# Optimization experiments

Hardware: AMD Instinct MI355X
Metric: run time of the kernel (lower is better)

Reference implementation:

```python
import jax, jax.numpy as jnp
import numpy as np

N_WIN = 7
DIM = 128
QK = 128
HEADS = 8
TOPK = 4


def _win(x, n_win):
    # (N, H, W, C) -> (N, n_win*n_win, h, w, C)
    N, H, W, C = x.shape
    h, w = H // n_win, W // n_win
    return x.reshape(N, n_win, h, n_win, w, C).transpose(0, 1, 3, 2, 4, 5).reshape(N, n_win * n_win, h, w, C)


def _unwin(x, n_win):
    # (N, p2, h, w, C) -> (N, H, W, C)
    N, p2, h, w, C = x.shape
    return x.reshape(N, n_win, n_win, h, w, C).transpose(0, 1, 3, 2, 4, 5).reshape(N, n_win * h, n_win * w, C)


def _dwconv(img_nhwc, k, b):
    # depthwise 3x3, SAME padding (LePE)
    x = img_nhwc.transpose(0, 3, 1, 2)
    y = jax.lax.conv_general_dilated(x, k, (1, 1), 'SAME',
                                     dimension_numbers=('NCHW', 'OIHW', 'NCHW'),
                                     feature_group_count=k.shape[0])
    y = y + b[None, :, None, None]
    return y.transpose(0, 2, 3, 1)


def _branch(xw, W, b):
    # xw: (N, p2, h, w, C); QKV linear + pixel/window-level views
    qkv = xw @ W + b
    q, kv = qkv[..., :QK], qkv[..., QK:]
    N, p2, h, w, _ = q.shape
    q_pix = q.reshape(N, p2, h * w, QK)
    kv_pix = kv.reshape(N, p2, h * w, QK + DIM)  # identity kv_down
    q_win = q.mean((2, 3))
    k_win = kv[..., :QK].mean((2, 3))
    return q_pix, kv_pix, q_win, k_win, kv


def _route(q_win, k_win, scale):
    # non-differentiable routing (detach) with Identity emb
    q = jax.lax.stop_gradient(q_win)
    k = jax.lax.stop_gradient(k_win)
    logit = (q * scale) @ k.transpose(0, 2, 1)  # (N, p2, p2)
    top_val, top_idx = jax.lax.top_k(logit, TOPK)
    r_weight = jax.nn.softmax(top_val, axis=-1)  # unused (mul_weight='none')
    return r_weight, top_idx


def _gather(kv_pix, idx):
    # kv_pix: (N, p2, w2, c), idx: (N, p2, K) -> (N, p2, K, w2, c)
    N = kv_pix.shape[0]
    bidx = jnp.arange(N)[:, None, None]
    return kv_pix[bidx, idx]


def _heads_q(q):
    # (N, p2, w2, m*c) -> (N, p2, m, w2, c)
    N, p2, w2, _ = q.shape
    return q.reshape(N, p2, w2, HEADS, -1).transpose(0, 1, 3, 2, 4)


def _heads_kv(kv):
    # (N, p2, K, w2, m*c) -> (N, p2, m, K*w2, c)
    N, p2, K, w2, _ = kv.shape
    return kv.reshape(N, p2, K, w2, HEADS, -1).transpose(0, 1, 4, 2, 3, 5).reshape(N, p2, HEADS, K * w2, -1)


def setup_inputs() -> dict:
    key = jax.random.key(0)
    ks = jax.random.split(key, 6)
    N, H, W = 8, 56, 56
    return {
        'x': jax.random.normal(ks[0], (N, H, W, DIM), jnp.float32),
        'y': jax.random.normal(ks[1], (N, H, W, DIM), jnp.float32),
        'w_qkv_x': jax.random.normal(ks[2], (DIM, 2 * QK + DIM), jnp.float32) * 0.02,
        'b_qkv_x': jnp.zeros((2 * QK + DIM,), jnp.float32),
        'w_qkv_y': jax.random.normal(ks[3], (DIM, 2 * QK + DIM), jnp.float32) * 0.02,
        'b_qkv_y': jnp.zeros((2 * QK + DIM,), jnp.float32),
        'w_lepe_x': jax.random.normal(ks[4], (DIM, 1, 3, 3), jnp.float32) * 0.1,
        'b_lepe_x': jnp.zeros((DIM,), jnp.float32),
        'w_lepe_y': jax.random.normal(ks[5], (DIM, 1, 3, 3), jnp.float32) * 0.1,
        'b_lepe_y': jnp.zeros((DIM,), jnp.float32),
    }


def reference(x, y, w_qkv_x, b_qkv_x, w_qkv_y, b_qkv_y, w_lepe_x, b_lepe_x, w_lepe_y, b_lepe_y):
    scale = QK ** (-0.5)
    N, H, W, C = x.shape
    h, w = H // N_WIN, W // N_WIN
    xw = _win(x, N_WIN)
    yw = _win(y, N_WIN)

    qx_pix, kvx_pix, qx_win, kx_win, kvx = _branch(xw, w_qkv_x, b_qkv_x)
    qy_pix, kvy_pix, qy_win, ky_win, kvy = _branch(yw, w_qkv_y, b_qkv_y)

    lepe_x = _dwconv(_unwin(kvx[..., QK:], N_WIN), w_lepe_x, b_lepe_x)
    lepe_y = _dwconv(_unwin(kvy[..., QK:], N_WIN), w_lepe_y, b_lepe_y)

    _, rx_idx = _route(qx_win, kx_win, scale)
    _, ry_idx = _route(qy_win, ky_win, scale)

    kvx_sel = _gather(kvx_pix, rx_idx)  # (N, p2, K, w2, QK+DIM)
    kvy_sel = _gather(kvy_pix, ry_idx)

    kx_sel, vx_sel = _heads_kv(kvx_sel[..., :QK]), _heads_kv(kvx_sel[..., QK:])
    ky_sel, vy_sel = _heads_kv(kvy_sel[..., :QK]), _heads_kv(kvy_sel[..., QK:])
    qx = _heads_q(qx_pix)
    qy = _heads_q(qy_pix)

    attn_x = jax.nn.softmax(jnp.einsum('bpmqc,bpmkc->bpmqk', qx * scale, kx_sel), axis=-1)
    attn_y = jax.nn.softmax(jnp.einsum('bpmqc,bpmkc->bpmqk', qy * scale, ky_sel), axis=-1)

    # cross attention: x-output uses y's attention weights on x's values, and vice versa
    out_x = jnp.einsum('bpmqk,bpmkc->bpmqc', attn_y, vx_sel)
    out_y = jnp.einsum('bpmqk,bpmkc->bpmqc', attn_x, vy_sel)

    p2 = N_WIN * N_WIN
    out_x = out_x.transpose(0, 1, 3, 2, 4).reshape(N, p2, h, w, DIM)
    out_y = out_y.transpose(0, 1, 3, 2, 4).reshape(N, p2, h, w, DIM)
    out_x = _unwin(out_x, N_WIN) + lepe_x
    out_y = _unwin(out_y, N_WIN) + lepe_y
    return (out_x, out_y)
```

## Files before the change

### kernel.cpp

```cpp
#include <hip/hip_runtime.h>

#define HWD 56
#define NWIN 7
#define P2 49
#define CIN 128
#define COUT 384
#define NB 8
#define SCALE 0.08838834764831843f

typedef __attribute__((ext_vector_type(8))) short bf16x8;
typedef __attribute__((ext_vector_type(4))) float f32x4;
typedef __attribute__((ext_vector_type(8))) unsigned short u16x8;
typedef unsigned short ushort_t;

#if __has_builtin(__builtin_amdgcn_mfma_f32_16x16x16bf16_1k)
#define HAVE_MFMA16 1
typedef __attribute__((ext_vector_type(4))) short bf16x4;
#endif

__device__ inline unsigned short f2bf(float f) {
  unsigned int u = __float_as_uint(f);
  unsigned int r = (u + 0x7fffu + ((u >> 16) & 1u)) >> 16;
  return (unsigned short)r;
}
__device__ inline float bf2f(unsigned short b) {
  return __uint_as_float(((unsigned int)b) << 16);
}

__global__ __launch_bounds__(256) void meanproj_kernel(
    const float* __restrict__ xin, const float* __restrict__ yin,
    const float* __restrict__ Wx, const float* __restrict__ Bx,
    const float* __restrict__ Wy, const float* __restrict__ By,
    ushort_t* __restrict__ xbfx, ushort_t* __restrict__ xbfy,
    ushort_t* __restrict__ Wtx, ushort_t* __restrict__ Wty,
    float* __restrict__ qwx, float* __restrict__ kwx,
    float* __restrict__ qwy, float* __restrict__ kwy)
{
  const int n = blockIdx.x, p = blockIdx.y, br = blockIdx.z;
  const float* X  = br ? yin : xin;
  const float* W  = br ? Wy  : Wx;
  const float* Bv = br ? By  : Bx;
  ushort_t* xb = (br ? xbfy : xbfx) + (size_t)(n * P2 + p) * 64 * CIN;
  ushort_t* Wt = br ? Wty : Wtx;
  float* qw = br ? qwy : qwx;
  float* kw = br ? kwy : kwx;

  __shared__ float smf[8][132];
  __shared__ float mxs[128];
  const int t = threadIdx.x;
  const int wr = p / NWIN, wc = p % NWIN;
  const int ch4 = (t & 31) * 4, pg = t >> 5;

  const float* Xrow = X + (((size_t)n * HWD + wr * 8 + pg) * HWD + wc * 8) * CIN;
  float4 s4 = {0.f, 0.f, 0.f, 0.f};
#pragma unroll
  for (int i = 0; i < 8; ++i) {
    float4 v = *(const float4*)&Xrow[i * CIN + ch4];
    s4.x += v.x; s4.y += v.y; s4.z += v.z; s4.w += v.w;
    ushort4 o = {f2bf(v.x), f2bf(v.y), f2bf(v.z), f2bf(v.w)};
    *(ushort4*)&xb[(pg * 8 + i) * CIN + ch4] = o;
  }
  *(float4*)&smf[pg][ch4] = s4;
  __syncthreads();
  if (t < 128) {
    float s = 0.f;
#pragma unroll
    for (int g = 0; g < 8; ++g) s += smf[g][t];
    mxs[t] = s * (1.f / 64.f);
  }
  __syncthreads();

  float acc = Bv[t];
#pragma unroll 8
  for (int k = 0; k < 128; ++k) acc = fmaf(mxs[k], W[(size_t)k * COUT + t], acc);
  if (t < 128) qw[(n * P2 + p) * 128 + t] = acc;
  else         kw[(n * P2 + p) * 128 + (t - 128)] = acc;

  if (p == 0) {
    for (int e = t; e < 48 * 128; e += 256) {
      int c = n * 48 + (e >> 7), k = e & 127;
      Wt[(size_t)c * 128 + k] = f2bf(W[(size_t)k * COUT + c]);
    }
  }
}

__global__ __launch_bounds__(256) void route_kernel(
    const float* __restrict__ qwx, const float* __restrict__ kwx,
    const float* __restrict__ qwy, const float* __restrict__ kwy,
    int* __restrict__ idxx, int* __restrict__ idxy)
{
  const int br = blockIdx.x, n = blockIdx.y;
  const float* qw = br ? qwy : qwx;
  const float* kw = br ? kwy : kwx;
  int* idx = br ? idxy : idxx;

  __shared__ float qs[P2][128];
  __shared__ float ks[P2][128];
  __shared__ float ls[P2][52];
  const int t = threadIdx.x;
  for (int e = t; e < P2 * 128; e += 256) {
    qs[e >> 7][e & 127] = qw[(size_t)n * P2 * 128 + e];
    ks[e >> 7][e & 127] = kw[(size_t)n * P2 * 128 + e];
  }
  __syncthreads();
  for (int pair = t; pair < P2 * P2; pair += 256) {
    int r = pair / P2, j = pair % P2;
    float d = 0.f;
#pragma unroll
    for (int c4 = 0; c4 < 32; ++c4) {
      float4 a = *(const float4*)&qs[r][c4 * 4];
      float4 b = *(const float4*)&ks[j][c4 * 4];
      d = fmaf(a.x, b.x, d); d = fmaf(a.y, b.y, d);
      d = fmaf(a.z, b.z, d); d = fmaf(a.w, b.w, d);
    }
    ls[r][j] = d;
  }
  __syncthreads();
  const int lane = t & 63, wv = t >> 6;
  for (int row = wv; row < P2; row += 4) {
    float v = (lane < P2) ? ls[row][lane] : -1e30f;
    int out4[4];
#pragma unroll
    for (int sel = 0; sel < 4; ++sel) {
      float m = v;
#pragma unroll
      for (int msk = 1; msk < 64; msk <<= 1) m = fmaxf(m, __shfl_xor(m, msk));
      unsigned long long b = __ballot(v == m);
      int bi = __ffsll((unsigned long long)b) - 1;
      out4[sel] = bi;
      if (lane == bi) v = -1e30f;
    }
    if (lane == 0) {
      int4 o = {out4[0], out4[1], out4[2], out4[3]};
      *(int4*)&idx[((size_t)n * P2 + row) * 4] = o;
    }
  }
}

#define XS 136
__global__ __launch_bounds__(256) void qkv_gemm_kernel(
    const ushort_t* __restrict__ xbfx, const ushort_t* __restrict__ xbfy,
    const ushort_t* __restrict__ Wtx, const ushort_t* __restrict__ Wty,
    const float* __restrict__ Bx, const float* __restrict__ By,
    ushort_t* __restrict__ Qpx, ushort_t* __restrict__ Qpy,
    ushort_t* __restrict__ Kpx, ushort_t* __restrict__ Kpy,
    ushort_t* __restrict__ Vcx, ushort_t* __restrict__ Vcy,
    ushort_t* __restrict__ Vpx, ushort_t* __restrict__ Vpy)
{
  const int n = blockIdx.x, p = blockIdx.y, br = blockIdx.z;
  const ushort_t* Xw = (br ? xbfy : xbfx) + (size_t)(n * P2 + p) * 64 * CIN;
  const ushort_t* Wt = br ? Wty : Wtx;
  const float* Bv = br ? By : Bx;
  ushort_t* Qp = br ? Qpy : Qpx;
  ushort_t* Kp = br ? Kpy : Kpx;
  ushort_t* Vc = br ? Vcy : Vcx;
  ushort_t* Vp = br ? Vpy : Vpx;

  __shared__ ushort_t a_s[64 * XS];

  const int t = threadIdx.x;
#pragma unroll
  for (int it = 0; it < 4; ++it) {
    int e = it * 256 + t;
    int row = e >> 4, c8 = (e & 15) * 8;
    *(u16x8*)&a_s[row * XS + c8] = *(const u16x8*)&Xw[row * 128 + c8];
  }
  __syncthreads();

  const int wv = t >> 6, lane = t & 63, qd = lane >> 4, m16 = lane & 15;
  const ushort_t* Wb = Wt + (size_t)(wv * 96) * 128;

  f32x4 acc[4][6];
#pragma unroll
  for (int i = 0; i < 4; ++i)
#pragma unroll
    for (int j = 0; j < 6; ++j) acc[i][j] = (f32x4){0.f, 0.f, 0.f, 0.f};

#pragma unroll
  for (int ks = 0; ks < 4; ++ks) {
    bf16x8 af[4], bfw[6];
#pragma unroll
    for (int fi = 0; fi < 4; ++fi)
      af[fi] = *(const bf16x8*)&a_s[(fi * 16 + m16) * XS + ks * 32 + qd * 8];
#pragma unroll
    for (int fj = 0; fj < 6; ++fj)
      bfw[fj] = *(const bf16x8*)&Wb[(size_t)(fj * 16 + m16) * 128 + ks * 32 + qd * 8];
#pragma unroll
    for (int fi = 0; fi < 4; ++fi)
#pragma unroll
      for (int fj = 0; fj < 6; ++fj)
        acc[fi][fj] = __builtin_amdgcn_mfma_f32_16x16x32_bf16(bfw[fj], af[fi], acc[fi][fj], 0, 0, 0);
  }

  const size_t wb = (size_t)(n * P2 + p) * 8;
#pragma unroll
  for (int fj = 0; fj < 6; ++fj) {
    const int ch = wv * 96 + fj * 16 + qd * 4;
    float4 b4 = *(const float4*)&Bv[ch];
    const int isQ = ch < 128, isK = (ch >= 128) && (ch < 256);
    const float scl = isQ ? SCALE : 1.0f;
    const int lch = ch & 127, h = lch >> 4, chlo = lch & 15;
#pragma unroll
    for (int fi = 0; fi < 4; ++fi) {
      int pix = fi * 16 + m16;
      float v0 = (acc[fi][fj][0] + b4.x) * scl, v1 = (acc[fi][fj][1] + b4.y) * scl;
      float v2 = (acc[fi][fj][2] + b4.z) * scl, v3 = (acc[fi][fj][3] + b4.w) * scl;
      ushort4 st = {f2bf(v0), f2bf(v1), f2bf(v2), f2bf(v3)};
      if (isQ) {
        *(ushort4*)&Qp[((wb + h) * 64 + pix) * 16 + chlo] = st;
      } else if (isK) {
        *(ushort4*)&Kp[((wb + h) * 64 + pix) * 16 + chlo] = st;
      } else {
        *(ushort4*)&Vp[((wb + h) * 64 + pix) * 16 + chlo] = st;
        size_t cb = ((wb + h) * 16 + chlo) * 64 + pix;
        Vc[cb] = st.x; Vc[cb + 64] = st.y; Vc[cb + 128] = st.z; Vc[cb + 192] = st.w;
      }
    }
  }
}

__global__ __launch_bounds__(256) void attn_kernel(
    const ushort_t* __restrict__ Qpx, const ushort_t* __restrict__ Qpy,
    const ushort_t* __restrict__ Kpx, const ushort_t* __restrict__ Kpy,
    const ushort_t* __restrict__ Vcx, const ushort_t* __restrict__ Vcy,
    const ushort_t* __restrict__ Vpx, const ushort_t* __restrict__ Vpy,
    const int* __restrict__ idxx, const int* __restrict__ idxy,
    const float* __restrict__ wlx, const float* __restrict__ blx,
    const float* __restrict__ wly, const float* __restrict__ bly,
    float* __restrict__ dout)
{
  const int n = blockIdx.x, p = blockIdx.y, z = blockIdx.z;
  const int h = z >> 1, dir = z & 1;
  const ushort_t* Qp = dir ? Qpy : Qpx;
  const ushort_t* Kp = dir ? Kpy : Kpx;
  const ushort_t* Vc = dir ? Vcx : Vcy;
  const ushort_t* Vp = dir ? Vpx : Vpy;
  const int* idxK = dir ? idxy : idxx;
  const int* idxV = dir ? idxx : idxy;
  const float* wl = dir ? wlx : wly;
  const float* bl = dir ? blx : bly;
  const size_t OUTHALF = (size_t)NB * HWD * HWD * CIN;
  float* outp = dout + (dir ? 0 : OUTHALF);

  __shared__ float halo[100 * 20];
  __shared__ float wls[160];

  const int t = threadIdx.x;
  const int wv = t >> 6;
  const int wr = p / NWIN, wc = p % NWIN;

  const int4 kidx = *(const int4*)&idxK[((size_t)n * P2 + p) * 4];
  const int4 vidx = *(const int4*)&idxV[((size_t)n * P2 + p) * 4];
  const int kw4[4] = {kidx.x, kidx.y, kidx.z, kidx.w};
  const int vw4[4] = {vidx.x, vidx.y, vidx.z, vidx.w};

  if (t < 200) {
    int hp = t >> 1, hf = t & 1;
    int A = wr * 8 - 1 + (int)((unsigned)hp / 10u);
    int B = wc * 8 - 1 + (int)((unsigned)hp % 10u);
    f32x4 f0 = {0.f, 0.f, 0.f, 0.f}, f1 = {0.f, 0.f, 0.f, 0.f};
    if ((unsigned)A < (unsigned)HWD && (unsigned)B < (unsigned)HWD) {
      int gw = (A >> 3) * NWIN + (B >> 3);
      int pix = (A & 7) * 8 + (B & 7);
      u16x8 vv = *(const u16x8*)&Vp[(((size_t)(n * P2 + gw) * 8 + h) * 64 + pix) * 16 + hf * 8];
      f0[0] = bf2f(vv[0]); f0[1] = bf2f(vv[1]); f0[2] = bf2f(vv[2]); f0[3] = bf2f(vv[3]);
      f1[0] = bf2f(vv[4]); f1[1] = bf2f(vv[5]); f1[2] = bf2f(vv[6]); f1[3] = bf2f(vv[7]);
    }
    *(f32x4*)&halo[hp * 20 + hf * 8] = f0;
    *(f32x4*)&halo[hp * 20 + hf * 8 + 4] = f1;
  }
  if (t < 160) {
    int row = t >> 4, c = t & 15;
    wls[t] = (row < 9) ? wl[(h * 16 + c) * 9 + row] : bl[h * 16 + c];
  }

  const int lane = t & 63, qd = lane >> 4, m16 = lane & 15;
  const f32x4 zf = {0.f, 0.f, 0.f, 0.f};
  const ushort_t* Qw = Qp + ((size_t)(n * P2 + p) * 8 + h) * 1024;

  f32x4 s[8][2];
#if HAVE_MFMA16
  bf16x4 qf = *(const bf16x4*)&Qw[(wv * 16 + m16) * 16 + qd * 4];
#pragma unroll
  for (int c = 0; c < 8; ++c) {
    const ushort_t* Kw = Kp + ((size_t)(n * P2 + kw4[c >> 1]) * 8 + h) * 1024;
    int lk = (c & 1) * 32;
    bf16x4 kf0 = *(const bf16x4*)&Kw[(lk + m16) * 16 + qd * 4];
    bf16x4 kf1 = *(const bf16x4*)&Kw[(lk + 16 + m16) * 16 + qd * 4];
    s[c][0] = __builtin_amdgcn_mfma_f32_16x16x16bf16_1k(kf0, qf, zf, 0, 0, 0);
    s[c][1] = __builtin_amdgcn_mfma_f32_16x16x16bf16_1k(kf1, qf, zf, 0, 0, 0);
  }
#else
  bf16x8 qf = (bf16x8)(short)0;
  if (qd < 2) qf = *(const bf16x8*)&Qw[(wv * 16 + m16) * 16 + qd * 8];
#pragma unroll
  for (int c = 0; c < 8; ++c) {
    const ushort_t* Kw = Kp + ((size_t)(n * P2 + kw4[c >> 1]) * 8 + h) * 1024;
    int lk = (c & 1) * 32;
    bf16x8 kf0 = (bf16x8)(short)0, kf1 = (bf16x8)(short)0;
    if (qd < 2) {
      kf0 = *(const bf16x8*)&Kw[(lk + m16) * 16 + qd * 8];
      kf1 = *(const bf16x8*)&Kw[(lk + 16 + m16) * 16 + qd * 8];
    }
    s[c][0] = __builtin_amdgcn_mfma_f32_16x16x32_bf16(kf0, qf, zf, 0, 0, 0);
    s[c][1] = __builtin_amdgcn_mfma_f32_16x16x32_bf16(kf1, qf, zf, 0, 0, 0);
  }
#endif

  float m = -1e30f;
#pragma unroll
  for (int c = 0; c < 8; ++c)
#pragma unroll
    for (int hh = 0; hh < 2; ++hh)
#pragma unroll
      for (int rr = 0; rr < 4; ++rr) m = fmaxf(m, s[c][hh][rr]);
  m = fmaxf(m, __shfl_xor(m, 16));
  m = fmaxf(m, __shfl_xor(m, 32));
  float l = 0.f;
#pragma unroll
  for (int c = 0; c < 8; ++c)
#pragma unroll
    for (int hh = 0; hh < 2; ++hh)
#pragma unroll
      for (int rr = 0; rr < 4; ++rr) {
        float e = __expf(s[c][hh][rr] - m);
        s[c][hh][rr] = e;
        l += e;
      }
  l += __shfl_xor(l, 16);
  l += __shfl_xor(l, 32);
  const float inv = 1.f / l;

  f32x4 oacc = {0.f, 0.f, 0.f, 0.f};
#pragma unroll
  for (int c = 0; c < 8; ++c) {
    int pk[4];
#pragma unroll
    for (int rr = 0; rr < 4; ++rr)
      pk[rr] = (int)((unsigned int)f2bf(s[c][0][rr]) | ((unsigned int)f2bf(s[c][1][rr]) << 16));
    u16x8 pfu;
#pragma unroll
    for (int j = 0; j < 8; ++j) {
      int srcl = (((qd & 1) * 2 + (j >> 2)) << 4) + m16;
      int w = __shfl(pk[j & 3], srcl);
      pfu[j] = (qd < 2) ? (unsigned short)(w & 0xffff) : (unsigned short)((unsigned)w >> 16);
    }
    const ushort_t* Vw = Vc + ((size_t)(n * P2 + vw4[c >> 1]) * 8 + h) * 1024;
    bf16x8 vtf = *(const bf16x8*)&Vw[m16 * 64 + (c & 1) * 32 + qd * 8];
    oacc = __builtin_amdgcn_mfma_f32_16x16x32_bf16(vtf, *(bf16x8*)&pfu, oacc, 0, 0, 0);
  }

  __syncthreads();

  const int pix = wv * 16 + m16;
  const int pa = pix >> 3, pb = pix & 7;

  f32x4 lep = *(const f32x4*)&wls[144 + qd * 4];
#pragma unroll
  for (int di = 0; di < 3; ++di)
#pragma unroll
    for (int dj = 0; dj < 3; ++dj) {
      f32x4 hv = *(const f32x4*)&halo[((pa + di) * 10 + pb + dj) * 20 + qd * 4];
      f32x4 wt4 = *(const f32x4*)&wls[(di * 3 + dj) * 16 + qd * 4];
#pragma unroll
      for (int rr = 0; rr < 4; ++rr) lep[rr] = fmaf(hv[rr], wt4[rr], lep[rr]);
    }

  const int ga = wr * 8 + pa, gb = wc * 8 + pb;
  float4 o = {oacc[0] * inv + lep[0], oacc[1] * inv + lep[1],
              oacc[2] * inv + lep[2], oacc[3] * inv + lep[3]};
  *(float4*)&outp[(((size_t)n * HWD + ga) * HWD + gb) * CIN + h * 16 + qd * 4] = o;
}

extern "C" void kernel_launch(void* const* d_in, const int* in_sizes, int n_in,
                              void* d_out, int out_size, void* d_ws, size_t ws_size,
                              hipStream_t stream) {
  const float* x        = (const float*)d_in[0];
  const float* y        = (const float*)d_in[1];
  const float* w_qkv_x  = (const float*)d_in[2];
  const float* b_qkv_x  = (const float*)d_in[3];
  const float* w_qkv_y  = (const float*)d_in[4];
  const float* b_qkv_y  = (const float*)d_in[5];
  const float* w_lepe_x = (const float*)d_in[6];
  const float* b_lepe_x = (const float*)d_in[7];
  const float* w_lepe_y = (const float*)d_in[8];
  const float* b_lepe_y = (const float*)d_in[9];
  float* out = (float*)d_out;

  const size_t hb_sz  = (size_t)NB * P2 * 8 * 64 * 16;
  const size_t xbf_sz = (size_t)NB * P2 * 64 * CIN;
  const size_t wt_sz  = (size_t)COUT * CIN;
  const size_t win_sz = (size_t)NB * P2 * 128;

  ushort_t* base = (ushort_t*)d_ws;
  ushort_t* Qpx = base;            ushort_t* Qpy = Qpx + hb_sz;
  ushort_t* Kpx = Qpy + hb_sz;     ushort_t* Kpy = Kpx + hb_sz;
  ushort_t* Vcx = Kpy + hb_sz;     ushort_t* Vcy = Vcx + hb_sz;
  ushort_t* Vpx = Vcy + hb_sz;     ushort_t* Vpy = Vpx + hb_sz;
  ushort_t* xbfx = Vpy + hb_sz;    ushort_t* xbfy = xbfx + xbf_sz;
  ushort_t* Wtx  = xbfy + xbf_sz;  ushort_t* Wty  = Wtx + wt_sz;
  float* qwx = (float*)(Wty + wt_sz);
  float* kwx = qwx + win_sz;
  float* qwy = kwx + win_sz;
  float* kwy = qwy + win_sz;
  int* idxx = (int*)(kwy + win_sz);
  int* idxy = idxx + NB * P2 * 4;

  meanproj_kernel<<<dim3(NB, P2, 2), 256, 0, stream>>>(
      x, y, w_qkv_x, b_qkv_x, w_qkv_y, b_qkv_y, xbfx, xbfy, Wtx, Wty,
      qwx, kwx, qwy, kwy);
  route_kernel<<<dim3(2, NB), 256, 0, stream>>>(qwx, kwx, qwy, kwy, idxx, idxy);
  qkv_gemm_kernel<<<dim3(NB, P2, 2), 256, 0, stream>>>(
      xbfx, xbfy, Wtx, Wty, b_qkv_x, b_qkv_y,
      Qpx, Qpy, Kpx, Kpy, Vcx, Vcy, Vpx, Vpy);
  attn_kernel<<<dim3(NB, P2, 16), 256, 0, stream>>>(
      Qpx, Qpy, Kpx, Kpy, Vcx, Vcy, Vpx, Vpy, idxx, idxy,
      w_lepe_x, b_lepe_x, w_lepe_y, b_lepe_y, out);
}
```

Measured before the change: 221.0 us.

## Fuse mean-projection into QKV GEMM, split weight transpose, parallelize routing, LDS P relayout

Folds the window-mean and routing projection into the QKV GEMM kernel, which now reads fp32 inputs straight into LDS as bf16 and no longer round-trips an xbf buffer through global memory. The weight transpose moves into a small separate kernel. Routing is reworked to one wavefront per window row with shuffle reductions, giving many more blocks. In attention, the cross-lane shuffle repack of P into the MFMA operand layout is replaced by an LDS staging buffer, and bf16 packing uses a packed-convert builtin when it exists. The costs are more LDS per attention block, with possible occupancy loss, and an extra kernel launch.

```diff
diff --git a/kernel.cpp b/kernel.cpp
--- a/kernel.cpp
+++ b/kernel.cpp
@@ -26,144 +26,81 @@
 __device__ inline float bf2f(unsigned short b) {
   return __uint_as_float(((unsigned int)b) << 16);
 }
-
-__global__ __launch_bounds__(256) void meanproj_kernel(
+__device__ inline unsigned int pk2bf(float a, float b) {
+#if __has_builtin(__builtin_amdgcn_cvt_pk_bf16_f32)
+  auto r = __builtin_amdgcn_cvt_pk_bf16_f32(a, b);
+  return *(unsigned int*)&r;
+#else
+  return (unsigned int)f2bf(a) | ((unsigned int)f2bf(b) << 16);
+#endif
+}
+
+__global__ __launch_bounds__(128) void wt_kernel(
+    const float* __restrict__ Wx, const float* __restrict__ Wy,
+    ushort_t* __restrict__ Wtx, ushort_t* __restrict__ Wty)
+{
+  const int br = blockIdx.y;
+  const float* W = br ? Wy : Wx;
+  ushort_t* Wt = br ? Wty : Wtx;
+  const int c = blockIdx.x * 128 + threadIdx.x;
+  for (int k8 = 0; k8 < 128; k8 += 8) {
+    u16x8 buf;
+#pragma unroll
+    for (int i = 0; i < 8; ++i) buf[i] = f2bf(W[(size_t)(k8 + i) * COUT + c]);
+    *(u16x8*)&Wt[(size_t)c * 128 + k8] = buf;
+  }
+}
+
+#define XS 136
+__global__ __launch_bounds__(256) void fused_gemm_kernel(
     const float* __restrict__ xin, const float* __restrict__ yin,
-    const float* __restrict__ Wx, const float* __restrict__ Bx,
-    const float* __restrict__ Wy, const float* __restrict__ By,
-    ushort_t* __restrict__ xbfx, ushort_t* __restrict__ xbfy,
-    ushort_t* __restrict__ Wtx, ushort_t* __restrict__ Wty,
+    const float* __restrict__ Wx, const float* __restrict__ Wy,
+    const ushort_t* __restrict__ Wtx, const ushort_t* __restrict__ Wty,
+    const float* __restrict__ Bx, const float* __restrict__ By,
+    ushort_t* __restrict__ Qpx, ushort_t* __restrict__ Qpy,
+    ushort_t* __restrict__ Kpx, ushort_t* __restrict__ Kpy,
+    ushort_t* __restrict__ Vcx, ushort_t* __restrict__ Vcy,
+    ushort_t* __restrict__ Vpx, ushort_t* __restrict__ Vpy,
     float* __restrict__ qwx, float* __restrict__ kwx,
     float* __restrict__ qwy, float* __restrict__ kwy)
 {
   const int n = blockIdx.x, p = blockIdx.y, br = blockIdx.z;
   const float* X  = br ? yin : xin;
   const float* W  = br ? Wy  : Wx;
-  const float* Bv = br ? By  : Bx;
-  ushort_t* xb = (br ? xbfy : xbfx) + (size_t)(n * P2 + p) * 64 * CIN;
-  ushort_t* Wt = br ? Wty : Wtx;
-  float* qw = br ? qwy : qwx;
-  float* kw = br ? kwy : kwx;
-
-  __shared__ float smf[8][132];
-  __shared__ float mxs[128];
-  const int t = threadIdx.x;
-  const int wr = p / NWIN, wc = p % NWIN;
-  const int ch4 = (t & 31) * 4, pg = t >> 5;
-
-  const float* Xrow = X + (((size_t)n * HWD + wr * 8 + pg) * HWD + wc * 8) * CIN;
-  float4 s4 = {0.f, 0.f, 0.f, 0.f};
-#pragma unroll
-  for (int i = 0; i < 8; ++i) {
-    float4 v = *(const float4*)&Xrow[i * CIN + ch4];
-    s4.x += v.x; s4.y += v.y; s4.z += v.z; s4.w += v.w;
-    ushort4 o = {f2bf(v.x), f2bf(v.y), f2bf(v.z), f2bf(v.w)};
-    *(ushort4*)&xb[(pg * 8 + i) * CIN + ch4] = o;
-  }
-  *(float4*)&smf[pg][ch4] = s4;
-  __syncthreads();
-  if (t < 128) {
-    float s = 0.f;
-#pragma unroll
-    for (int g = 0; g < 8; ++g) s += smf[g][t];
-    mxs[t] = s * (1.f / 64.f);
-  }
-  __syncthreads();
-
-  float acc = Bv[t];
-#pragma unroll 8
-  for (int k = 0; k < 128; ++k) acc = fmaf(mxs[k], W[(size_t)k * COUT + t], acc);
-  if (t < 128) qw[(n * P2 + p) * 128 + t] = acc;
-  else         kw[(n * P2 + p) * 128 + (t - 128)] = acc;
-
-  if (p == 0) {
-    for (int e = t; e < 48 * 128; e += 256) {
-      int c = n * 48 + (e >> 7), k = e & 127;
-      Wt[(size_t)c * 128 + k] = f2bf(W[(size_t)k * COUT + c]);
-    }
-  }
-}
-
-__global__ __launch_bounds__(256) void route_kernel(
-    const float* __restrict__ qwx, const float* __restrict__ kwx,
-    const float* __restrict__ qwy, const float* __restrict__ kwy,
-    int* __restrict__ idxx, int* __restrict__ idxy)
-{
-  const int br = blockIdx.x, n = blockIdx.y;
-  const float* qw = br ? qwy : qwx;
-  const float* kw = br ? kwy : kwx;
-  int* idx = br ? idxy : idxx;
-
-  __shared__ float qs[P2][128];
-  __shared__ float ks[P2][128];
-  __shared__ float ls[P2][52];
-  const int t = threadIdx.x;
-  for (int e = t; e < P2 * 128; e += 256) {
-    qs[e >> 7][e & 127] = qw[(size_t)n * P2 * 128 + e];
-    ks[e >> 7][e & 127] = kw[(size_t)n * P2 * 128 + e];
-  }
-  __syncthreads();
-  for (int pair = t; pair < P2 * P2; pair += 256) {
-    int r = pair / P2, j = pair % P2;
-    float d = 0.f;
-#pragma unroll
-    for (int c4 = 0; c4 < 32; ++c4) {
-      float4 a = *(const float4*)&qs[r][c4 * 4];
-      float4 b = *(const float4*)&ks[j][c4 * 4];
-      d = fmaf(a.x, b.x, d); d = fmaf(a.y, b.y, d);
-      d = fmaf(a.z, b.z, d); d = fmaf(a.w, b.w, d);
-    }
-    ls[r][j] = d;
-  }
-  __syncthreads();
-  const int lane = t & 63, wv = t >> 6;
-  for (int row = wv; row < P2; row += 4) {
-    float v = (lane < P2) ? ls[row][lane] : -1e30f;
-    int out4[4];
-#pragma unroll
-    for (int sel = 0; sel < 4; ++sel) {
-      float m = v;
-#pragma unroll
-      for (int msk = 1; msk < 64; msk <<= 1) m = fmaxf(m, __shfl_xor(m, msk));
-      unsigned long long b = __ballot(v == m);
-      int bi = __ffsll((unsigned long long)b) - 1;
-      out4[sel] = bi;
-      if (lane == bi) v = -1e30f;
-    }
-    if (lane == 0) {
-      int4 o = {out4[0], out4[1], out4[2], out4[3]};
-      *(int4*)&idx[((size_t)n * P2 + row) * 4] = o;
-    }
-  }
-}
-
-#define XS 136
-__global__ __launch_bounds__(256) void qkv_gemm_kernel(
-    const ushort_t* __restrict__ xbfx, const ushort_t* __restrict__ xbfy,
-    const ushort_t* __restrict__ Wtx, const ushort_t* __restrict__ Wty,
-    const float* __restrict__ Bx, const float* __restrict__ By,
-    ushort_t* __restrict__ Qpx, ushort_t* __restrict__ Qpy,
-    ushort_t* __restrict__ Kpx, ushort_t* __restrict__ Kpy,
-    ushort_t* __restrict__ Vcx, ushort_t* __restrict__ Vcy,
-    ushort_t* __restrict__ Vpx, ushort_t* __restrict__ Vpy)
-{
-  const int n = blockIdx.x, p = blockIdx.y, br = blockIdx.z;
-  const ushort_t* Xw = (br ? xbfy : xbfx) + (size_t)(n * P2 + p) * 64 * CIN;
   const ushort_t* Wt = br ? Wty : Wtx;
   const float* Bv = br ? By : Bx;
   ushort_t* Qp = br ? Qpy : Qpx;
   ushort_t* Kp = br ? Kpy : Kpx;
   ushort_t* Vc = br ? Vcy : Vcx;
   ushort_t* Vp = br ? Vpy : Vpx;
+  float* qw = br ? qwy : qwx;
+  float* kw = br ? kwy : kwx;
 
   __shared__ ushort_t a_s[64 * XS];
+  __shared__ float smf[8][132];
+  __shared__ float mxs[128];
 
   const int t = threadIdx.x;
-#pragma unroll
-  for (int it = 0; it < 4; ++it) {
-    int e = it * 256 + t;
-    int row = e >> 4, c8 = (e & 15) * 8;
-    *(u16x8*)&a_s[row * XS + c8] = *(const u16x8*)&Xw[row * 128 + c8];
+  const int wr = p / NWIN, wc = p % NWIN;
+  const int pr = t >> 5, ch4 = (t & 31) * 4;
+
+  float4 s4 = {0.f, 0.f, 0.f, 0.f};
+#pragma unroll
+  for (int i = 0; i < 8; ++i) {
+    const float* Xrow = X + (((size_t)n * HWD + wr * 8 + i) * HWD + wc * 8) * CIN;
+    float4 v = *(const float4*)&Xrow[pr * CIN + ch4];
+    s4.x += v.x; s4.y += v.y; s4.z += v.z; s4.w += v.w;
+    unsigned int lo = pk2bf(v.x, v.y), hi = pk2bf(v.z, v.w);
+    uint2 st = {lo, hi};
+    *(uint2*)&a_s[(i * 8 + pr) * XS + ch4] = st;
+  }
+  *(float4*)&smf[pr][ch4] = s4;
+  __syncthreads();
+  if (t < 128) {
+    float s = 0.f;
+#pragma unroll
+    for (int g = 0; g < 8; ++g) s += smf[g][t];
+    mxs[t] = s * (1.f / 64.f);
   }
   __syncthreads();
 
@@ -205,20 +142,70 @@
       int pix = fi * 16 + m16;
       float v0 = (acc[fi][fj][0] + b4.x) * scl, v1 = (acc[fi][fj][1] + b4.y) * scl;
       float v2 = (acc[fi][fj][2] + b4.z) * scl, v3 = (acc[fi][fj][3] + b4.w) * scl;
-      ushort4 st = {f2bf(v0), f2bf(v1), f2bf(v2), f2bf(v3)};
+      unsigned int lo = pk2bf(v0, v1), hi = pk2bf(v2, v3);
+      uint2 st = {lo, hi};
       if (isQ) {
-        *(ushort4*)&Qp[((wb + h) * 64 + pix) * 16 + chlo] = st;
+        *(uint2*)&Qp[((wb + h) * 64 + pix) * 16 + chlo] = st;
       } else if (isK) {
-        *(ushort4*)&Kp[((wb + h) * 64 + pix) * 16 + chlo] = st;
+        *(uint2*)&Kp[((wb + h) * 64 + pix) * 16 + chlo] = st;
       } else {
-        *(ushort4*)&Vp[((wb + h) * 64 + pix) * 16 + chlo] = st;
+        *(uint2*)&Vp[((wb + h) * 64 + pix) * 16 + chlo] = st;
         size_t cb = ((wb + h) * 16 + chlo) * 64 + pix;
-        Vc[cb] = st.x; Vc[cb + 64] = st.y; Vc[cb + 128] = st.z; Vc[cb + 192] = st.w;
+        Vc[cb]       = (ushort_t)(lo & 0xffff);
+        Vc[cb + 64]  = (ushort_t)(lo >> 16);
+        Vc[cb + 128] = (ushort_t)(hi & 0xffff);
+        Vc[cb + 192] = (ushort_t)(hi >> 16);
       }
     }
   }
-}
-
+
+  float accp = Bv[t];
+#pragma unroll 8
+  for (int k = 0; k < 128; ++k) accp = fmaf(mxs[k], W[(size_t)k * COUT + t], accp);
+  if (t < 128) qw[(n * P2 + p) * 128 + t] = accp;
+  else         kw[(n * P2 + p) * 128 + (t - 128)] = accp;
+}
+
+__global__ __launch_bounds__(64) void route_kernel(
+    const float* __restrict__ qwx, const float* __restrict__ kwx,
+    const float* __restrict__ qwy, const float* __restrict__ kwy,
+    int* __restrict__ idxx, int* __restrict__ idxy)
+{
+  const int r = blockIdx.x, n = blockIdx.y, br = blockIdx.z;
+  const float* qw = br ? qwy : qwx;
+  const float* kw = br ? kwy : kwx;
+  int* idx = br ? idxy : idxx;
+
+  const int lane = threadIdx.x;
+  float2 q2 = *(const float2*)&qw[((size_t)n * P2 + r) * 128 + lane * 2];
+
+  float v = -1e30f;
+  for (int j = 0; j < P2; ++j) {
+    float2 k2 = *(const float2*)&kw[((size_t)n * P2 + j) * 128 + lane * 2];
+    float d = fmaf(q2.x, k2.x, q2.y * k2.y);
+#pragma unroll
+    for (int msk = 1; msk < 64; msk <<= 1) d += __shfl_xor(d, msk);
+    if (lane == j) v = d;
+  }
+
+  int out4[4];
+#pragma unroll
+  for (int sel = 0; sel < 4; ++sel) {
+    float m = v;
+#pragma unroll
+    for (int msk = 1; msk < 64; msk <<= 1) m = fmaxf(m, __shfl_xor(m, msk));
+    unsigned long long b = __ballot(v == m);
+    int bi = __ffsll(b) - 1;
+    out4[sel] = bi;
+    if (lane == bi) v = -1e30f;
+  }
+  if (lane == 0) {
+    int4 o = {out4[0], out4[1], out4[2], out4[3]};
+    *(int4*)&idx[((size_t)n * P2 + r) * 4] = o;
+  }
+}
+
+#define PBS 264
 __global__ __launch_bounds__(256) void attn_kernel(
     const ushort_t* __restrict__ Qpx, const ushort_t* __restrict__ Qpy,
     const ushort_t* __restrict__ Kpx, const ushort_t* __restrict__ Kpy,
@@ -244,6 +231,7 @@
 
   __shared__ float halo[100 * 20];
   __shared__ float wls[160];
+  __shared__ ushort_t pb[4 * 16 * PBS];
 
   const int t = threadIdx.x;
   const int wv = t >> 6;
@@ -331,20 +319,19 @@
   l += __shfl_xor(l, 32);
   const float inv = 1.f / l;
 
+  ushort_t* pbw = pb + wv * 16 * PBS + m16 * PBS;
+#pragma unroll
+  for (int c = 0; c < 8; ++c) {
+    uint2 lo = {pk2bf(s[c][0][0], s[c][0][1]), pk2bf(s[c][0][2], s[c][0][3])};
+    uint2 hi = {pk2bf(s[c][1][0], s[c][1][1]), pk2bf(s[c][1][2], s[c][1][3])};
+    *(uint2*)&pbw[c * 32 + qd * 4] = lo;
+    *(uint2*)&pbw[c * 32 + qd * 4 + 16] = hi;
+  }
+
   f32x4 oacc = {0.f, 0.f, 0.f, 0.f};
 #pragma unroll
   for (int c = 0; c < 8; ++c) {
-    int pk[4];
-#pragma unroll
-    for (int rr = 0; rr < 4; ++rr)
-      pk[rr] = (int)((unsigned int)f2bf(s[c][0][rr]) | ((unsigned int)f2bf(s[c][1][rr]) << 16));
-    u16x8 pfu;
-#pragma unroll
-    for (int j = 0; j < 8; ++j) {
-      int srcl = (((qd & 1) * 2 + (j >> 2)) << 4) + m16;
-      int w = __shfl(pk[j & 3], srcl);
-      pfu[j] = (qd < 2) ? (unsigned short)(w & 0xffff) : (unsigned short)((unsigned)w >> 16);
-    }
+    u16x8 pfu = *(const u16x8*)&pbw[c * 32 + qd * 8];
     const ushort_t* Vw = Vc + ((size_t)(n * P2 + vw4[c >> 1]) * 8 + h) * 1024;
     bf16x8 vtf = *(const bf16x8*)&Vw[m16 * 64 + (c & 1) * 32 + qd * 8];
     oacc = __builtin_amdgcn_mfma_f32_16x16x32_bf16(vtf, *(bf16x8*)&pfu, oacc, 0, 0, 0);
@@ -353,20 +340,20 @@
   __syncthreads();
 
   const int pix = wv * 16 + m16;
-  const int pa = pix >> 3, pb = pix & 7;
+  const int pa = pix >> 3, pb2 = pix & 7;
 
   f32x4 lep = *(const f32x4*)&wls[144 + qd * 4];
 #pragma unroll
   for (int di = 0; di < 3; ++di)
 #pragma unroll
     for (int dj = 0; dj < 3; ++dj) {
-      f32x4 hv = *(const f32x4*)&halo[((pa + di) * 10 + pb + dj) * 20 + qd * 4];
+      f32x4 hv = *(const f32x4*)&halo[((pa + di) * 10 + pb2 + dj) * 20 + qd * 4];
       f32x4 wt4 = *(const f32x4*)&wls[(di * 3 + dj) * 16 + qd * 4];
 #pragma unroll
       for (int rr = 0; rr < 4; ++rr) lep[rr] = fmaf(hv[rr], wt4[rr], lep[rr]);
     }
 
-  const int ga = wr * 8 + pa, gb = wc * 8 + pb;
+  const int ga = wr * 8 + pa, gb = wc * 8 + pb2;
   float4 o = {oacc[0] * inv + lep[0], oacc[1] * inv + lep[1],
               oacc[2] * inv + lep[2], oacc[3] * inv + lep[3]};
   *(float4*)&outp[(((size_t)n * HWD + ga) * HWD + gb) * CIN + h * 16 + qd * 4] = o;
@@ -388,7 +375,6 @@
   float* out = (float*)d_out;
 
   const size_t hb_sz  = (size_t)NB * P2 * 8 * 64 * 16;
-  const size_t xbf_sz = (size_t)NB * P2 * 64 * CIN;
   const size_t wt_sz  = (size_t)COUT * CIN;
   const size_t win_sz = (size_t)NB * P2 * 128;
 
@@ -397,8 +383,7 @@
   ushort_t* Kpx = Qpy + hb_sz;     ushort_t* Kpy = Kpx + hb_sz;
   ushort_t* Vcx = Kpy + hb_sz;     ushort_t* Vcy = Vcx + hb_sz;
   ushort_t* Vpx = Vcy + hb_sz;     ushort_t* Vpy = Vpx + hb_sz;
-  ushort_t* xbfx = Vpy + hb_sz;    ushort_t* xbfy = xbfx + xbf_sz;
-  ushort_t* Wtx  = xbfy + xbf_sz;  ushort_t* Wty  = Wtx + wt_sz;
+  ushort_t* Wtx = Vpy + hb_sz;     ushort_t* Wty = Wtx + wt_sz;
   float* qwx = (float*)(Wty + wt_sz);
   float* kwx = qwx + win_sz;
   float* qwy = kwx + win_sz;
@@ -406,13 +391,11 @@
   int* idxx = (int*)(kwy + win_sz);
   int* idxy = idxx + NB * P2 * 4;
 
-  meanproj_kernel<<<dim3(NB, P2, 2), 256, 0, stream>>>(
-      x, y, w_qkv_x, b_qkv_x, w_qkv_y, b_qkv_y, xbfx, xbfy, Wtx, Wty,
-      qwx, kwx, qwy, kwy);
-  route_kernel<<<dim3(2, NB), 256, 0, stream>>>(qwx, kwx, qwy, kwy, idxx, idxy);
-  qkv_gemm_kernel<<<dim3(NB, P2, 2), 256, 0, stream>>>(
-      xbfx, xbfy, Wtx, Wty, b_qkv_x, b_qkv_y,
-      Qpx, Qpy, Kpx, Kpy, Vcx, Vcy, Vpx, Vpy);
+  wt_kernel<<<dim3(3, 2), 128, 0, stream>>>(w_qkv_x, w_qkv_y, Wtx, Wty);
+  fused_gemm_kernel<<<dim3(NB, P2, 2), 256, 0, stream>>>(
+      x, y, w_qkv_x, w_qkv_y, Wtx, Wty, b_qkv_x, b_qkv_y,
+      Qpx, Qpy, Kpx, Kpy, Vcx, Vcy, Vpx, Vpy, qwx, kwx, qwy, kwy);
+  route_kernel<<<dim3(P2, NB, 2), 64, 0, stream>>>(qwx, kwx, qwy, kwy, idxx, idxy);
   attn_kernel<<<dim3(NB, P2, 16), 256, 0, stream>>>(
       Qpx, Qpy, Kpx, Kpy, Vcx, Vcy, Vpx, Vpy, idxx, idxy,
       w_lepe_x, b_lepe_x, w_lepe_y, b_lepe_y, out);
```

Measured after the change: 199.1 us. 1.11x faster.
